# Optimization experiments

Hardware: AMD Instinct MI355X
Metric: run time of the kernel (lower is better)

## Reference

```python
import jax, jax.numpy as jnp
import numpy as np

N, E, B = 50000, 400000, 8
ND, ED, H, L = 32, 16, 128, 3

def setup_inputs() -> dict:
    key = jax.random.key(0)
    ks = jax.random.split(key, 32)
    s = 0.05
    inp = {
        'x': jax.random.normal(ks[0], (N, ND), jnp.float32),
        'edge_attr': jax.random.normal(ks[1], (E, ED), jnp.float32),
        'global_feature': jax.random.normal(ks[2], (B, 1), jnp.float32),
        'edge_index': jax.random.randint(ks[3], (2, E), 0, N, jnp.int64),
        'batch': jnp.sort(jax.random.randint(ks[4], (N,), 0, B, jnp.int64)),
        # embeddings
        'Wn': jax.random.normal(ks[5], (ND, H), jnp.float32) * s,
        'bn': jnp.zeros((H,), jnp.float32),
        'We': jax.random.normal(ks[6], (ED, H), jnp.float32) * s,
        'be': jnp.zeros((H,), jnp.float32),
        'Wg': jax.random.normal(ks[7], (1, H), jnp.float32) * s,
        'bg': jnp.zeros((H,), jnp.float32),
        # message-passing layers (stacked over L)
        'mW1': jax.random.normal(ks[8], (L, 3 * H, H), jnp.float32) * s,
        'mb1': jnp.zeros((L, H), jnp.float32),
        'mW2': jax.random.normal(ks[9], (L, H, H), jnp.float32) * s,
        'mb2': jnp.zeros((L, H), jnp.float32),
        'uW1': jax.random.normal(ks[10], (L, 2 * H, H), jnp.float32) * s,
        'ub1': jnp.zeros((L, H), jnp.float32),
        'uW2': jax.random.normal(ks[11], (L, H, H), jnp.float32) * s,
        'ub2': jnp.zeros((L, H), jnp.float32),
        # readout MLP
        'rW1': jax.random.normal(ks[12], (2 * H, H), jnp.float32) * s,
        'rb1': jnp.zeros((H,), jnp.float32),
        'rW2': jax.random.normal(ks[13], (H, H // 2), jnp.float32) * s,
        'rb2': jnp.zeros((H // 2,), jnp.float32),
        'rW3': jax.random.normal(ks[14], (H // 2, 1), jnp.float32) * s,
        'rb3': jnp.zeros((1,), jnp.float32),
    }
    return inp

def reference(x, edge_attr, global_feature, Wn, bn, We, be, Wg, bg,
              mW1, mb1, mW2, mb2, uW1, ub1, uW2, ub2,
              rW1, rb1, rW2, rb2, rW3, rb3, edge_index, batch):
    h = x @ Wn + bn                      # [N,H]
    e = edge_attr @ We + be              # [E,H]
    g = global_feature @ Wg + bg         # [B,H]
    src, dst = edge_index[0], edge_index[1]  # PyG: x_j=source, x_i=target, aggregate at target
    for l in range(L):
        m_in = jnp.concatenate([h[dst], h[src], e], axis=1)            # [E,3H]
        m = jax.nn.relu(m_in @ mW1[l] + mb1[l]) @ mW2[l] + mb2[l]       # [E,H]
        aggr = jax.ops.segment_sum(m, dst, num_segments=N)              # [N,H]
        u_in = jnp.concatenate([h, aggr], axis=1)                       # [N,2H]
        upd = jax.nn.relu(u_in @ uW1[l] + ub1[l]) @ uW2[l] + ub2[l]
        h = h + upd
    counts = jax.ops.segment_sum(jnp.ones((N,), h.dtype), batch, num_segments=B)
    pooled = jax.ops.segment_sum(h, batch, num_segments=B) / jnp.maximum(counts, 1.0)[:, None]
    final = jnp.concatenate([pooled, g], axis=1)                        # [B,2H]
    out = jax.nn.relu(final @ rW1 + rb1)
    out = jax.nn.relu(out @ rW2 + rb2)
    return out @ rW3 + rb3                                              # [B,1]
```

## Files before the change

kernel.cpp:

```cpp
#include <hip/hip_runtime.h>

#define NN 50000
#define NPAD 50048
#define NBLK 391
#define NE 400000
#define NBATCH 8
#define NDIM 32
#define EDIM 16
#define H 128
#define NLAYERS 3
#define CHUNK_ELEMS 4096
#define NODE_CHUNKS 24
#define ZW_CHUNK 8192
#define NSB 196

typedef __attribute__((ext_vector_type(8))) __bf16 bf16x8;
typedef __attribute__((ext_vector_type(16))) float f32x16;
typedef __attribute__((ext_vector_type(8))) short short8;
typedef __attribute__((ext_vector_type(2))) float v2f;

__device__ __forceinline__ void block_sync_lds() {
  asm volatile("s_waitcnt lgkmcnt(0)\ns_barrier" ::: "memory");
}
__device__ __forceinline__ v2f bf2f(unsigned u) {
  v2f r;
  r.x = __uint_as_float(u << 16);
  r.y = __uint_as_float(u & 0xffff0000u);
  return r;
}
__device__ __forceinline__ v2f fma2(float s, v2f w, v2f t) {
  v2f sv = {s, s};
  return __builtin_elementwise_fma(sv, w, t);
}

__global__ __launch_bounds__(128) void embed_nodes_kernel(
    const float* __restrict__ x, const float* __restrict__ Wn,
    const float* __restrict__ bn, __bf16* __restrict__ hb) {
  __shared__ float Ws[NDIM * H];
  __shared__ float xs[16 * NDIM];
  int j = threadIdx.x;
  int nbase = blockIdx.x * 16;
  for (int r = 0; r < NDIM; ++r) Ws[r * H + j] = Wn[r * H + j];
#pragma unroll
  for (int t = 0; t < 4; ++t) {
    int f = j + t * 128;
    xs[f] = x[nbase * NDIM + f];
  }
  __syncthreads();
  float b = bn[j];
  for (int nn = 0; nn < 16; ++nn) {
    float acc = b;
#pragma unroll
    for (int k = 0; k < NDIM; ++k)
      acc = fmaf(xs[nn * NDIM + k], Ws[k * H + j], acc);
    hb[(size_t)(nbase + nn) * H + j] = (__bf16)acc;
  }
}

__global__ __launch_bounds__(256) void degree_kernel(const int* __restrict__ ei,
                                                     int* __restrict__ deg) {
  int e = blockIdx.x * 256 + threadIdx.x;
  if (e < NE) atomicAdd(&deg[ei[NE + e]], 1);
}

__global__ __launch_bounds__(256) void scan1_kernel(const int* __restrict__ deg,
                                                    int* __restrict__ bsum) {
  __shared__ int ws[4];
  int i = blockIdx.x * 256 + threadIdx.x;
  int lane = threadIdx.x & 63, wid = threadIdx.x >> 6;
  int v = (i < NN) ? deg[i] : 0;
#pragma unroll
  for (int off = 32; off; off >>= 1) v += __shfl_down(v, off);
  if (lane == 0) ws[wid] = v;
  __syncthreads();
  if (threadIdx.x == 0) bsum[blockIdx.x] = ws[0] + ws[1] + ws[2] + ws[3];
}

__global__ __launch_bounds__(256) void scan2_kernel(const int* __restrict__ bsum,
                                                    int* __restrict__ boff) {
  __shared__ int s[256];
  int t = threadIdx.x;
  int v = (t < NSB) ? bsum[t] : 0;
  s[t] = v;
  __syncthreads();
  for (int off = 1; off < 256; off <<= 1) {
    int u = (t >= off) ? s[t - off] : 0;
    __syncthreads();
    s[t] += u;
    __syncthreads();
  }
  if (t < NSB) boff[t] = s[t] - v;
}

__global__ __launch_bounds__(256) void scan3_kernel(const int* __restrict__ deg,
                                                    const int* __restrict__ boff,
                                                    int* __restrict__ cursor) {
  __shared__ int wsum[4], woff[4];
  int i = blockIdx.x * 256 + threadIdx.x;
  int lane = threadIdx.x & 63, wid = threadIdx.x >> 6;
  int orig = (i < NN) ? deg[i] : 0;
  int v = orig;
#pragma unroll
  for (int off = 1; off < 64; off <<= 1) {
    int u = __shfl_up(v, off);
    if (lane >= off) v += u;
  }
  if (lane == 63) wsum[wid] = v;
  __syncthreads();
  if (threadIdx.x == 0) {
    int r = 0;
#pragma unroll
    for (int w = 0; w < 4; ++w) {
      woff[w] = r;
      r += wsum[w];
    }
  }
  __syncthreads();
  if (i < NN) cursor[i] = (v - orig) + woff[wid] + boff[blockIdx.x];
}

__global__ __launch_bounds__(256) void scatter_kernel(
    const int* __restrict__ ei, int* __restrict__ cursor,
    int2* __restrict__ seSrt) {
  int e = blockIdx.x * 256 + threadIdx.x;
  if (e < NE) {
    int d = ei[NE + e];
    int pos = atomicAdd(&cursor[d], 1);
    seSrt[pos] = make_int2(ei[e], e);
  }
}

__global__ __launch_bounds__(256) void gather_eaF_kernel(
    const float* __restrict__ ea, const int2* __restrict__ seSrt,
    float* __restrict__ eaF) {
  int fl = blockIdx.x * 256 + threadIdx.x;
  if (fl < NE) {
    int e = seSrt[fl].y;
    const float4* ep = (const float4*)(ea + (size_t)e * EDIM);
    float4* op = (float4*)(eaF + (size_t)fl * EDIM);
#pragma unroll
    for (int q = 0; q < 4; ++q) op[q] = ep[q];
  }
}

__global__ __launch_bounds__(256) void precomp_zw_kernel(
    const float* __restrict__ mW1, __bf16* __restrict__ ZW) {
  int l = blockIdx.x / 8;
  int c = blockIdx.x % 8;
  int tid = threadIdx.x;
  const float* w1 = mW1 + (size_t)l * 384 * H;
  __bf16* dst = ZW + ((size_t)l * 8 + c) * ZW_CHUNK;
  for (int it = 0; it < 32; ++it) {
    int flat = it * 256 + tid;
    int j = flat & 7;
    int lane = (flat >> 3) & 63;
    int nt = (flat >> 9) & 7;
    int hilo = flat >> 12;
    int k = c * 16 + ((lane >> 5) << 3) + j;
    int n = nt * 32 + (lane & 31);
    float w = (n < 128) ? w1[(size_t)k * H + n]
                        : w1[(size_t)(128 + k) * H + (n - 128)];
    __bf16 hi = (__bf16)w;
    __bf16 lo = (__bf16)(w - (float)hi);
    dst[flat] = hilo ? lo : hi;
  }
}

__global__ __launch_bounds__(128) void precomp_wef_kernel(
    const float* __restrict__ mW1, const float* __restrict__ mb1,
    const float* __restrict__ We, const float* __restrict__ be,
    float* __restrict__ Wef, float* __restrict__ bm) {
  int l = blockIdx.x;
  int n = threadIdx.x;
  const float* w1 = mW1 + (size_t)l * 384 * H;
  float acc[EDIM];
#pragma unroll
  for (int i = 0; i < EDIM; ++i) acc[i] = 0.f;
  float accb = 0.f;
  for (int c = 0; c < H; ++c) {
    float wv = w1[(size_t)(256 + c) * H + n];
    accb = fmaf(be[c], wv, accb);
#pragma unroll
    for (int i = 0; i < EDIM; ++i)
      acc[i] = fmaf(We[i * H + c], wv, acc[i]);
  }
#pragma unroll
  for (int i = 0; i < EDIM; ++i)
    Wef[((size_t)l * EDIM + i) * H + n] = acc[i];
  bm[l * H + n] = mb1[l * H + n] + accb;
}

__global__ __launch_bounds__(128) void precomp_wu_kernel(
    const float* __restrict__ uW1, const float* __restrict__ mW2,
    const float* __restrict__ mb2, float* __restrict__ Wu,
    float* __restrict__ va) {
  int l = blockIdx.x / 257;
  int r = blockIdx.x % 257;
  int j = threadIdx.x;
  const float* u1 = uW1 + (size_t)l * 256 * H;
  if (r < 128) {
    Wu[((size_t)l * 256 + r) * H + j] = u1[(size_t)r * H + j];
  } else if (r < 256) {
    int i = r - 128;
    const float* m2 = mW2 + ((size_t)l * H + i) * H;
    float s = 0.f;
    for (int c = 0; c < H; ++c)
      s = fmaf(m2[c], u1[(size_t)(128 + c) * H + j], s);
    Wu[((size_t)l * 256 + r) * H + j] = s;
  } else {
    float s = 0.f;
    for (int c = 0; c < H; ++c)
      s = fmaf(mb2[l * H + c], u1[(size_t)(128 + c) * H + j], s);
    va[l * H + j] = s;
  }
}

__global__ __launch_bounds__(256) void precomp_wns_kernel(
    const float* __restrict__ Wu, const float* __restrict__ uW2,
    __bf16* __restrict__ WnS) {
  int l = blockIdx.x / NODE_CHUNKS;
  int c = blockIdx.x % NODE_CHUNKS;
  int tid = threadIdx.x;
  int nt = tid >> 6, lane = tid & 63;
  int n = nt * 32 + (lane & 31);
  int half = lane >> 5;
  __bf16* dst = WnS + ((size_t)l * NODE_CHUNKS + c) * CHUNK_ELEMS;
#pragma unroll
  for (int j = 0; j < 8; ++j) {
    float w;
    if (c < 16) {
      int k = c * 16 + half * 8 + j;
      w = Wu[((size_t)l * 256 + k) * H + n];
    } else {
      int k = (c - 16) * 16 + half * 8 + j;
      w = uW2[((size_t)l * H + k) * H + n];
    }
    __bf16 hi = (__bf16)w;
    __bf16 lo = (__bf16)(w - (float)hi);
    dst[((0 * 4 + nt) * 64 + lane) * 8 + j] = hi;
    dst[((1 * 4 + nt) * 64 + lane) * 8 + j] = lo;
  }
}

__global__ __launch_bounds__(256) void zdzs_kernel(
    const __bf16* __restrict__ hb, const __bf16* __restrict__ ZW,
    const float* __restrict__ bm, __bf16* __restrict__ z) {
  __shared__ __align__(16) __bf16 Bt[2][ZW_CHUNK];
  int tid = threadIdx.x;
  int wid = tid >> 6, lane = tid & 63, m = lane & 31, half = lane >> 5;
  int nb = blockIdx.x * 128;
  int row = nb + wid * 32 + m;
  const __bf16* aH = hb + (size_t)row * H + half * 8;
  const short8* gW = (const short8*)ZW;
  short8* sB0 = (short8*)&Bt[0][0];
  short8* sB1 = (short8*)&Bt[1][0];
#pragma unroll
  for (int q = 0; q < 4; ++q) sB0[tid + q * 256] = gW[tid + q * 256];
  short8 p0 = gW[1024 + tid], p1 = gW[1024 + tid + 256];
  short8 p2 = gW[1024 + tid + 512], p3 = gW[1024 + tid + 768];
  f32x16 acc[8];
#pragma unroll
  for (int nt = 0; nt < 8; ++nt)
#pragma unroll
    for (int r = 0; r < 16; ++r) acc[nt][r] = 0.f;
  bf16x8 a = *(const bf16x8*)aH;
  block_sync_lds();

  for (int s = 0; s < 8; ++s) {
    int buf = s & 1;
    bf16x8 na = a;
    if (s + 1 < 8) na = *(const bf16x8*)(aH + (s + 1) * 16);
    if (s + 1 < 8) {
      short8* sb = buf ? sB0 : sB1;
      sb[tid] = p0;
      sb[tid + 256] = p1;
      sb[tid + 512] = p2;
      sb[tid + 768] = p3;
      if (s + 2 < 8) {
        p0 = gW[(size_t)(s + 2) * 1024 + tid];
        p1 = gW[(size_t)(s + 2) * 1024 + tid + 256];
        p2 = gW[(size_t)(s + 2) * 1024 + tid + 512];
        p3 = gW[(size_t)(s + 2) * 1024 + tid + 768];
      }
    }
    const __bf16* bb = &Bt[buf][0];
#pragma unroll
    for (int nt = 0; nt < 8; ++nt) {
      bf16x8 bh = *(const bf16x8*)&bb[((0 * 8 + nt) * 64 + lane) * 8];
      bf16x8 bl = *(const bf16x8*)&bb[((1 * 8 + nt) * 64 + lane) * 8];
      acc[nt] = __builtin_amdgcn_mfma_f32_32x32x16_bf16(a, bh, acc[nt], 0, 0, 0);
      acc[nt] = __builtin_amdgcn_mfma_f32_32x32x16_bf16(a, bl, acc[nt], 0, 0, 0);
    }
    a = na;
    if (s + 1 < 8) block_sync_lds();
  }

  float bmv[4];
#pragma unroll
  for (int nt = 0; nt < 4; ++nt) bmv[nt] = bm[nt * 32 + m];
#pragma unroll
  for (int nt = 0; nt < 8; ++nt) {
    float bias = (nt < 4) ? bmv[nt] : 0.f;
#pragma unroll
    for (int r = 0; r < 16; ++r) {
      int rowi = (r & 3) + 8 * (r >> 2) + 4 * half;
      z[(size_t)(nb + wid * 32 + rowi) * 256 + nt * 32 + m] =
          (__bf16)(acc[nt][r] + bias);
    }
  }
}

__global__ __launch_bounds__(256) void edge_aggr_kernel(
    const __bf16* __restrict__ z, const int2* __restrict__ seSrt,
    const int* __restrict__ cend, const float* __restrict__ eaF,
    const float* __restrict__ WefL, __bf16* __restrict__ aggrB) {
  __shared__ float wefS[EDIM * H];
  int tid = threadIdx.x;
#pragma unroll
  for (int q = 0; q < 8; ++q) wefS[tid + q * 256] = WefL[tid + q * 256];
  __syncthreads();
  int node = blockIdx.x * 4 + (tid >> 6);
  int lane = tid & 63;
  int c0 = lane * 2;
  v2f wef[16];
#pragma unroll
  for (int k = 0; k < 16; ++k) wef[k] = *(const v2f*)(&wefS[k * H + c0]);
  int end = cend[node];
  int start = node ? cend[node - 1] : 0;
  v2f acc = {0.f, 0.f};
  if (start < end) {
    v2f zd = bf2f(*(const unsigned*)(z + (size_t)node * 256 + c0));
    int sArr[4];
#pragma unroll
    for (int p = 0; p < 4; ++p)
      if (start + p < end) sArr[p] = seSrt[start + p].x;
    for (int e0 = start; e0 < end; e0 += 4) {
      unsigned zsb[4];
      float4 ea0[4], ea1[4], ea2[4], ea3[4];
#pragma unroll
      for (int p = 0; p < 4; ++p) {
        if (e0 + p < end) {
          zsb[p] = *(const unsigned*)(z + (size_t)sArr[p] * 256 + 128 + c0);
          const float4* ep = (const float4*)(eaF + (size_t)(e0 + p) * EDIM);
          ea0[p] = ep[0]; ea1[p] = ep[1]; ea2[p] = ep[2]; ea3[p] = ep[3];
        }
      }
#pragma unroll
      for (int p = 0; p < 4; ++p)
        if (e0 + 4 + p < end) sArr[p] = seSrt[e0 + 4 + p].x;
#pragma unroll
      for (int p = 0; p < 4; ++p) {
        if (e0 + p < end) {
          v2f t = zd + bf2f(zsb[p]);
          t = fma2(ea0[p].x, wef[0], t);
          t = fma2(ea0[p].y, wef[1], t);
          t = fma2(ea0[p].z, wef[2], t);
          t = fma2(ea0[p].w, wef[3], t);
          t = fma2(ea1[p].x, wef[4], t);
          t = fma2(ea1[p].y, wef[5], t);
          t = fma2(ea1[p].z, wef[6], t);
          t = fma2(ea1[p].w, wef[7], t);
          t = fma2(ea2[p].x, wef[8], t);
          t = fma2(ea2[p].y, wef[9], t);
          t = fma2(ea2[p].z, wef[10], t);
          t = fma2(ea2[p].w, wef[11], t);
          t = fma2(ea3[p].x, wef[12], t);
          t = fma2(ea3[p].y, wef[13], t);
          t = fma2(ea3[p].z, wef[14], t);
          t = fma2(ea3[p].w, wef[15], t);
          acc.x += fmaxf(t.x, 0.f);
          acc.y += fmaxf(t.y, 0.f);
        }
      }
    }
  }
  union { __bf16 b[2]; unsigned u; } pk;
  pk.b[0] = (__bf16)acc.x;
  pk.b[1] = (__bf16)acc.y;
  *(unsigned*)(aggrB + (size_t)node * H + c0) = pk.u;
}

__global__ __launch_bounds__(256) void node_update_mfma_kernel(
    __bf16* __restrict__ hb, const __bf16* __restrict__ aggrB,
    const int* __restrict__ deg, const __bf16* __restrict__ WnS,
    const float* __restrict__ ub1, const float* __restrict__ va,
    const float* __restrict__ ub2) {
  __shared__ __align__(16) __bf16 Bt[2][CHUNK_ELEMS];
  __shared__ __bf16 hid[2][32][132];
  __shared__ float degS[64];
  int tid = threadIdx.x;
  int nb = blockIdx.x * 64;
  if (tid < 64) degS[tid] = (float)deg[nb + tid];
  int wid = tid >> 6, lane = tid & 63, m = lane & 31, half = lane >> 5;
  int rg = wid & 1;
  int nh = wid >> 1;
  int row = nb + rg * 32 + m;
  const __bf16* aHb = hb + (size_t)row * H + half * 8;
  const __bf16* aGb = aggrB + (size_t)row * H + half * 8;
  const short8* gW = (const short8*)WnS;
  short8* sB0 = (short8*)&Bt[0][0];
  short8* sB1 = (short8*)&Bt[1][0];
  sB0[tid] = gW[tid];
  sB0[tid + 256] = gW[tid + 256];
  short8 p0 = gW[512 + tid], p1 = gW[512 + tid + 256];
  float bv1[2], bva[2];
#pragma unroll
  for (int ntl = 0; ntl < 2; ++ntl) {
    int nt = nh * 2 + ntl;
    bv1[ntl] = ub1[nt * 32 + m];
    bva[ntl] = va[nt * 32 + m];
  }
  f32x16 acc[2];
#pragma unroll
  for (int ntl = 0; ntl < 2; ++ntl)
#pragma unroll
    for (int r = 0; r < 16; ++r) acc[ntl][r] = 0.f;
  bf16x8 acur = *(const bf16x8*)aHb;
  block_sync_lds();

  for (int s = 0; s < 16; ++s) {
    int buf = s & 1;
    bf16x8 anext = acur;
    if (s + 1 < 16) {
      int sp = s + 1;
      anext = (sp < 8) ? *(const bf16x8*)(aHb + sp * 16)
                       : *(const bf16x8*)(aGb + (sp - 8) * 16);
    }
    {
      short8* sb = buf ? sB0 : sB1;
      sb[tid] = p0;
      sb[tid + 256] = p1;
      if (s + 2 < NODE_CHUNKS) {
        p0 = gW[(size_t)(s + 2) * 512 + tid];
        p1 = gW[(size_t)(s + 2) * 512 + tid + 256];
      }
    }
    const __bf16* bb = &Bt[buf][0];
#pragma unroll
    for (int ntl = 0; ntl < 2; ++ntl) {
      int nt = nh * 2 + ntl;
      bf16x8 bh = *(const bf16x8*)&bb[((0 * 4 + nt) * 64 + lane) * 8];
      bf16x8 bl = *(const bf16x8*)&bb[((1 * 4 + nt) * 64 + lane) * 8];
      acc[ntl] = __builtin_amdgcn_mfma_f32_32x32x16_bf16(acur, bh, acc[ntl], 0, 0, 0);
      acc[ntl] = __builtin_amdgcn_mfma_f32_32x32x16_bf16(acur, bl, acc[ntl], 0, 0, 0);
    }
    acur = anext;
    block_sync_lds();
  }

#pragma unroll
  for (int ntl = 0; ntl < 2; ++ntl) {
    int nt = nh * 2 + ntl;
#pragma unroll
    for (int r = 0; r < 16; ++r) {
      int rowi = (r & 3) + 8 * (r >> 2) + 4 * half;
      float v = acc[ntl][r] + bv1[ntl] + degS[rg * 32 + rowi] * bva[ntl];
      hid[rg][rowi][nt * 32 + m] = (__bf16)fmaxf(v, 0.f);
      acc[ntl][r] = 0.f;
    }
  }
  block_sync_lds();

  for (int s = 16; s < NODE_CHUNKS; ++s) {
    int buf = s & 1;
    if (s + 1 < NODE_CHUNKS) {
      short8* sb = buf ? sB0 : sB1;
      sb[tid] = p0;
      sb[tid + 256] = p1;
      if (s + 2 < NODE_CHUNKS) {
        p0 = gW[(size_t)(s + 2) * 512 + tid];
        p1 = gW[(size_t)(s + 2) * 512 + tid + 256];
      }
    }
    bf16x8 ah = *(const bf16x8*)&hid[rg][m][(s - 16) * 16 + half * 8];
    const __bf16* bb = &Bt[buf][0];
#pragma unroll
    for (int ntl = 0; ntl < 2; ++ntl) {
      int nt = nh * 2 + ntl;
      bf16x8 bh = *(const bf16x8*)&bb[((0 * 4 + nt) * 64 + lane) * 8];
      bf16x8 bl = *(const bf16x8*)&bb[((1 * 4 + nt) * 64 + lane) * 8];
      acc[ntl] = __builtin_amdgcn_mfma_f32_32x32x16_bf16(ah, bh, acc[ntl], 0, 0, 0);
      acc[ntl] = __builtin_amdgcn_mfma_f32_32x32x16_bf16(ah, bl, acc[ntl], 0, 0, 0);
    }
    if (s + 1 < NODE_CHUNKS) block_sync_lds();
  }

#pragma unroll
  for (int ntl = 0; ntl < 2; ++ntl) {
    int nt = nh * 2 + ntl;
    float b2 = ub2[nt * 32 + m];
#pragma unroll
    for (int r = 0; r < 16; ++r) {
      int rowi = (r & 3) + 8 * (r >> 2) + 4 * half;
      size_t idx = (size_t)(nb + rg * 32 + rowi) * H + nt * 32 + m;
      float hv = (float)hb[idx];
      hb[idx] = (__bf16)(hv + acc[ntl][r] + b2);
    }
  }
}

__global__ __launch_bounds__(256) void pool_kernel(
    const __bf16* __restrict__ hb, const int* __restrict__ batch,
    float* __restrict__ pooled, int* __restrict__ counts) {
  __shared__ float pS[NBATCH * H];
  __shared__ int cS[NBATCH];
  int tid = threadIdx.x;
  for (int i = tid; i < NBATCH * H; i += 256) pS[i] = 0.f;
  if (tid < NBATCH) cS[tid] = 0;
  __syncthreads();
  int c = tid & 15;
  int r0 = tid >> 4;
  int nbase = blockIdx.x * 128;
  v2f acc4[4] = {{0.f, 0.f}, {0.f, 0.f}, {0.f, 0.f}, {0.f, 0.f}};
  int cnt = 0;
  int cur = -1;
#pragma unroll
  for (int i = 0; i < 8; ++i) {
    int n = nbase + i * 16 + r0;
    if (n >= NN) break;
    int b = batch[n];
    if (b != cur) {
      if (cur >= 0) {
#pragma unroll
        for (int q = 0; q < 4; ++q) {
          atomicAdd(&pS[cur * H + c * 8 + q * 2], acc4[q].x);
          atomicAdd(&pS[cur * H + c * 8 + q * 2 + 1], acc4[q].y);
          acc4[q].x = 0.f;
          acc4[q].y = 0.f;
        }
        if (c == 0) atomicAdd(&cS[cur], cnt);
        cnt = 0;
      }
      cur = b;
    }
    uint4 v = *(const uint4*)(hb + (size_t)n * H + c * 8);
    acc4[0] += bf2f(v.x);
    acc4[1] += bf2f(v.y);
    acc4[2] += bf2f(v.z);
    acc4[3] += bf2f(v.w);
    cnt++;
  }
  if (cur >= 0) {
#pragma unroll
    for (int q = 0; q < 4; ++q) {
      atomicAdd(&pS[cur * H + c * 8 + q * 2], acc4[q].x);
      atomicAdd(&pS[cur * H + c * 8 + q * 2 + 1], acc4[q].y);
    }
    if (c == 0) atomicAdd(&cS[cur], cnt);
  }
  __syncthreads();
  for (int i = tid; i < NBATCH * H; i += 256) {
    float v = pS[i];
    if (v != 0.f) unsafeAtomicAdd(&pooled[i], v);
  }
  if (tid < NBATCH) {
    int cv = cS[tid];
    if (cv) atomicAdd(&counts[tid], cv);
  }
}

__global__ __launch_bounds__(128) void readout_kernel(
    const float* __restrict__ pooled, const int* __restrict__ counts,
    const float* __restrict__ gf, const float* __restrict__ Wg,
    const float* __restrict__ bg, const float* __restrict__ rW1,
    const float* __restrict__ rb1, const float* __restrict__ rW2,
    const float* __restrict__ rb2, const float* __restrict__ rW3,
    const float* __restrict__ rb3, float* __restrict__ out) {
  __shared__ float fin[256];
  __shared__ float t1[128];
  __shared__ float t2[64];
  int j = threadIdx.x;
  int b = blockIdx.x;
  float cnt = (float)counts[b];
  if (cnt < 1.f) cnt = 1.f;
  fin[j] = pooled[b * H + j] / cnt;
  fin[H + j] = fmaf(gf[b], Wg[j], bg[j]);
  __syncthreads();
  float a = rb1[j];
  for (int k = 0; k < 256; ++k) a = fmaf(fin[k], rW1[k * H + j], a);
  t1[j] = fmaxf(a, 0.f);
  __syncthreads();
  if (j < 64) {
    float a2 = rb2[j];
    for (int k = 0; k < 128; ++k) a2 = fmaf(t1[k], rW2[k * 64 + j], a2);
    t2[j] = fmaxf(a2, 0.f);
  }
  __syncthreads();
  if (j < 64) {
    float p = t2[j] * rW3[j];
#pragma unroll
    for (int off = 32; off; off >>= 1) p += __shfl_down(p, off);
    if (j == 0) out[b] = p + rb3[0];
  }
}

extern "C" void kernel_launch(void* const* d_in, const int* in_sizes, int n_in,
                              void* d_out, int out_size, void* d_ws, size_t ws_size,
                              hipStream_t stream) {
  const float* x   = (const float*)d_in[0];
  const float* ea  = (const float*)d_in[1];
  const float* gf  = (const float*)d_in[2];
  const int*   ei  = (const int*)d_in[3];
  const int*   bat = (const int*)d_in[4];
  const float* Wn  = (const float*)d_in[5];
  const float* bn  = (const float*)d_in[6];
  const float* We  = (const float*)d_in[7];
  const float* be  = (const float*)d_in[8];
  const float* Wg  = (const float*)d_in[9];
  const float* bg  = (const float*)d_in[10];
  const float* mW1 = (const float*)d_in[11];
  const float* mb1 = (const float*)d_in[12];
  const float* mW2 = (const float*)d_in[13];
  const float* mb2 = (const float*)d_in[14];
  const float* uW1 = (const float*)d_in[15];
  const float* ub1 = (const float*)d_in[16];
  const float* uW2 = (const float*)d_in[17];
  const float* ub2 = (const float*)d_in[18];
  const float* rW1 = (const float*)d_in[19];
  const float* rb1 = (const float*)d_in[20];
  const float* rW2 = (const float*)d_in[21];
  const float* rb2 = (const float*)d_in[22];
  const float* rW3 = (const float*)d_in[23];
  const float* rb3 = (const float*)d_in[24];

  char* p = (char*)d_ws;
  __bf16* hb     = (__bf16*)p; p += (size_t)NPAD * H * 2;
  __bf16* aggrB  = (__bf16*)p; p += (size_t)NPAD * H * 2;
  __bf16* z      = (__bf16*)p; p += (size_t)NPAD * 256 * 2;
  float*  eaF    = (float*)p;  p += (size_t)NE * EDIM * 4;
  int2*   seSrt  = (int2*)p;   p += (size_t)NE * 8;
  __bf16* ZW     = (__bf16*)p; p += (size_t)NLAYERS * 8 * ZW_CHUNK * 2;
  __bf16* WnS    = (__bf16*)p; p += (size_t)NLAYERS * NODE_CHUNKS * CHUNK_ELEMS * 2;
  float*  Wef    = (float*)p;  p += (size_t)NLAYERS * EDIM * H * 4;
  float*  bm     = (float*)p;  p += (size_t)NLAYERS * H * 4;
  float*  Wu     = (float*)p;  p += (size_t)NLAYERS * 256 * H * 4;
  float*  va     = (float*)p;  p += (size_t)NLAYERS * H * 4;
  int*    deg    = (int*)p;    p += (size_t)NPAD * 4;
  int*    cursor = (int*)p;    p += (size_t)NPAD * 4;
  int*    bsum   = (int*)p;    p += 256 * 4;
  int*    boff   = (int*)p;    p += 256 * 4;
  float*  pooled = (float*)p;  p += (size_t)NBATCH * H * 4;
  int*    counts = (int*)p;    p += 64;

  hipMemsetAsync(deg, 0, (size_t)NPAD * 4, stream);
  hipMemsetAsync(cursor, 0, (size_t)NPAD * 4, stream);
  hipMemsetAsync(pooled, 0, (size_t)NBATCH * H * 4, stream);
  hipMemsetAsync(counts, 0, 64, stream);

  embed_nodes_kernel<<<NN / 16, 128, 0, stream>>>(x, Wn, bn, hb);
  degree_kernel<<<(NE + 255) / 256, 256, 0, stream>>>(ei, deg);
  scan1_kernel<<<NSB, 256, 0, stream>>>(deg, bsum);
  scan2_kernel<<<1, 256, 0, stream>>>(bsum, boff);
  scan3_kernel<<<NSB, 256, 0, stream>>>(deg, boff, cursor);
  scatter_kernel<<<(NE + 255) / 256, 256, 0, stream>>>(ei, cursor, seSrt);
  gather_eaF_kernel<<<(NE + 255) / 256, 256, 0, stream>>>(ea, seSrt, eaF);
  precomp_zw_kernel<<<NLAYERS * 8, 256, 0, stream>>>(mW1, ZW);
  precomp_wef_kernel<<<NLAYERS, 128, 0, stream>>>(mW1, mb1, We, be, Wef, bm);
  precomp_wu_kernel<<<NLAYERS * 257, 128, 0, stream>>>(uW1, mW2, mb2, Wu, va);
  precomp_wns_kernel<<<NLAYERS * NODE_CHUNKS, 256, 0, stream>>>(Wu, uW2, WnS);

  for (int l = 0; l < NLAYERS; ++l) {
    zdzs_kernel<<<NBLK, 256, 0, stream>>>(
        hb, ZW + (size_t)l * 8 * ZW_CHUNK, bm + (size_t)l * H, z);
    edge_aggr_kernel<<<NPAD / 4, 256, 0, stream>>>(
        z, seSrt, cursor, eaF, Wef + (size_t)l * EDIM * H, aggrB);
    node_update_mfma_kernel<<<NPAD / 64, 256, 0, stream>>>(
        hb, aggrB, deg, WnS + (size_t)l * NODE_CHUNKS * CHUNK_ELEMS,
        ub1 + (size_t)l * H, va + (size_t)l * H, ub2 + (size_t)l * H);
  }

  pool_kernel<<<NPAD / 128, 256, 0, stream>>>(hb, bat, pooled, counts);
  readout_kernel<<<NBATCH, 128, 0, stream>>>(pooled, counts, gf, Wg, bg, rW1,
                                             rb1, rW2, rb2, rW3, rb3,
                                             (float*)d_out);
}
```

Before: 584.5 us.

## Switch edge aggregation to edge-balanced waves with segmented atomic flush

Edge aggregation now gives each wave a fixed run of 64 dst-sorted edges instead of one destination node, so per-wave work is balanced regardless of node degree. Partial segments at a wave's edges are merged with float atomics into an fp32 aggregate buffer, which is zeroed with a memset every layer. The node update reads the fp32 aggregate and converts it to bf16 on load. This adds a memset, doubles the aggregate traffic and introduces atomics in exchange for removing the imbalance from variable degree.

```diff
diff --git a/kernel.cpp b/kernel.cpp
--- a/kernel.cpp
+++ b/kernel.cpp
@@ -13,6 +13,8 @@
 #define NODE_CHUNKS 24
 #define ZW_CHUNK 8192
 #define NSB 196
+#define EPW 64
+#define EAB 1563
 
 typedef __attribute__((ext_vector_type(8))) __bf16 bf16x8;
 typedef __attribute__((ext_vector_type(16))) float f32x16;
@@ -121,21 +123,22 @@
 
 __global__ __launch_bounds__(256) void scatter_kernel(
     const int* __restrict__ ei, int* __restrict__ cursor,
-    int2* __restrict__ seSrt) {
+    int2* __restrict__ sdSrt, int* __restrict__ eidSrt) {
   int e = blockIdx.x * 256 + threadIdx.x;
   if (e < NE) {
     int d = ei[NE + e];
     int pos = atomicAdd(&cursor[d], 1);
-    seSrt[pos] = make_int2(ei[e], e);
+    sdSrt[pos] = make_int2(ei[e], d);
+    eidSrt[pos] = e;
   }
 }
 
 __global__ __launch_bounds__(256) void gather_eaF_kernel(
-    const float* __restrict__ ea, const int2* __restrict__ seSrt,
+    const float* __restrict__ ea, const int* __restrict__ eidSrt,
     float* __restrict__ eaF) {
   int fl = blockIdx.x * 256 + threadIdx.x;
   if (fl < NE) {
-    int e = seSrt[fl].y;
+    int e = eidSrt[fl];
     const float4* ep = (const float4*)(ea + (size_t)e * EDIM);
     float4* op = (float4*)(eaF + (size_t)fl * EDIM);
 #pragma unroll
@@ -310,78 +313,85 @@
   }
 }
 
+__device__ __forceinline__ void flush_seg(float* __restrict__ aggrF, int d,
+                                          int c0, v2f acc, bool partial) {
+  if (partial) {
+    unsafeAtomicAdd(&aggrF[(size_t)d * H + c0], acc.x);
+    unsafeAtomicAdd(&aggrF[(size_t)d * H + c0 + 1], acc.y);
+  } else {
+    *(v2f*)(&aggrF[(size_t)d * H + c0]) = acc;
+  }
+}
+
 __global__ __launch_bounds__(256) void edge_aggr_kernel(
-    const __bf16* __restrict__ z, const int2* __restrict__ seSrt,
-    const int* __restrict__ cend, const float* __restrict__ eaF,
-    const float* __restrict__ WefL, __bf16* __restrict__ aggrB) {
+    const __bf16* __restrict__ z, const int2* __restrict__ sdSrt,
+    const float* __restrict__ eaF, const float* __restrict__ WefL,
+    float* __restrict__ aggrF) {
   __shared__ float wefS[EDIM * H];
   int tid = threadIdx.x;
 #pragma unroll
   for (int q = 0; q < 8; ++q) wefS[tid + q * 256] = WefL[tid + q * 256];
   __syncthreads();
-  int node = blockIdx.x * 4 + (tid >> 6);
   int lane = tid & 63;
   int c0 = lane * 2;
+  int wave = blockIdx.x * 4 + (tid >> 6);
+  int e0 = wave * EPW;
+  if (e0 >= NE) return;
   v2f wef[16];
 #pragma unroll
   for (int k = 0; k < 16; ++k) wef[k] = *(const v2f*)(&wefS[k * H + c0]);
-  int end = cend[node];
-  int start = node ? cend[node - 1] : 0;
+
+  int curD = sdSrt[e0].y;
+  v2f zdv = bf2f(*(const unsigned*)(z + (size_t)curD * 256 + c0));
   v2f acc = {0.f, 0.f};
-  if (start < end) {
-    v2f zd = bf2f(*(const unsigned*)(z + (size_t)node * 256 + c0));
-    int sArr[4];
-#pragma unroll
-    for (int p = 0; p < 4; ++p)
-      if (start + p < end) sArr[p] = seSrt[start + p].x;
-    for (int e0 = start; e0 < end; e0 += 4) {
-      unsigned zsb[4];
-      float4 ea0[4], ea1[4], ea2[4], ea3[4];
-#pragma unroll
-      for (int p = 0; p < 4; ++p) {
-        if (e0 + p < end) {
-          zsb[p] = *(const unsigned*)(z + (size_t)sArr[p] * 256 + 128 + c0);
-          const float4* ep = (const float4*)(eaF + (size_t)(e0 + p) * EDIM);
-          ea0[p] = ep[0]; ea1[p] = ep[1]; ea2[p] = ep[2]; ea3[p] = ep[3];
-        }
+  bool firstSeg = true;
+
+  for (int b = e0; b < e0 + EPW; b += 8) {
+    int2 sd[8];
+#pragma unroll
+    for (int p = 0; p < 8; ++p) sd[p] = sdSrt[b + p];
+    unsigned zsb[8];
+#pragma unroll
+    for (int p = 0; p < 8; ++p)
+      zsb[p] = *(const unsigned*)(z + (size_t)sd[p].x * 256 + 128 + c0);
+#pragma unroll
+    for (int p = 0; p < 8; ++p) {
+      if (sd[p].y != curD) {
+        flush_seg(aggrF, curD, c0, acc, firstSeg);
+        firstSeg = false;
+        acc.x = 0.f;
+        acc.y = 0.f;
+        curD = sd[p].y;
+        zdv = bf2f(*(const unsigned*)(z + (size_t)curD * 256 + c0));
       }
-#pragma unroll
-      for (int p = 0; p < 4; ++p)
-        if (e0 + 4 + p < end) sArr[p] = seSrt[e0 + 4 + p].x;
-#pragma unroll
-      for (int p = 0; p < 4; ++p) {
-        if (e0 + p < end) {
-          v2f t = zd + bf2f(zsb[p]);
-          t = fma2(ea0[p].x, wef[0], t);
-          t = fma2(ea0[p].y, wef[1], t);
-          t = fma2(ea0[p].z, wef[2], t);
-          t = fma2(ea0[p].w, wef[3], t);
-          t = fma2(ea1[p].x, wef[4], t);
-          t = fma2(ea1[p].y, wef[5], t);
-          t = fma2(ea1[p].z, wef[6], t);
-          t = fma2(ea1[p].w, wef[7], t);
-          t = fma2(ea2[p].x, wef[8], t);
-          t = fma2(ea2[p].y, wef[9], t);
-          t = fma2(ea2[p].z, wef[10], t);
-          t = fma2(ea2[p].w, wef[11], t);
-          t = fma2(ea3[p].x, wef[12], t);
-          t = fma2(ea3[p].y, wef[13], t);
-          t = fma2(ea3[p].z, wef[14], t);
-          t = fma2(ea3[p].w, wef[15], t);
-          acc.x += fmaxf(t.x, 0.f);
-          acc.y += fmaxf(t.y, 0.f);
-        }
-      }
-    }
-  }
-  union { __bf16 b[2]; unsigned u; } pk;
-  pk.b[0] = (__bf16)acc.x;
-  pk.b[1] = (__bf16)acc.y;
-  *(unsigned*)(aggrB + (size_t)node * H + c0) = pk.u;
+      const float4* ep = (const float4*)(eaF + (size_t)(b + p) * EDIM);
+      float4 a0 = ep[0], a1 = ep[1], a2 = ep[2], a3 = ep[3];
+      v2f t = zdv + bf2f(zsb[p]);
+      t = fma2(a0.x, wef[0], t);
+      t = fma2(a0.y, wef[1], t);
+      t = fma2(a0.z, wef[2], t);
+      t = fma2(a0.w, wef[3], t);
+      t = fma2(a1.x, wef[4], t);
+      t = fma2(a1.y, wef[5], t);
+      t = fma2(a1.z, wef[6], t);
+      t = fma2(a1.w, wef[7], t);
+      t = fma2(a2.x, wef[8], t);
+      t = fma2(a2.y, wef[9], t);
+      t = fma2(a2.z, wef[10], t);
+      t = fma2(a2.w, wef[11], t);
+      t = fma2(a3.x, wef[12], t);
+      t = fma2(a3.y, wef[13], t);
+      t = fma2(a3.z, wef[14], t);
+      t = fma2(a3.w, wef[15], t);
+      acc.x += fmaxf(t.x, 0.f);
+      acc.y += fmaxf(t.y, 0.f);
+    }
+  }
+  flush_seg(aggrF, curD, c0, acc, true);
 }
 
 __global__ __launch_bounds__(256) void node_update_mfma_kernel(
-    __bf16* __restrict__ hb, const __bf16* __restrict__ aggrB,
+    __bf16* __restrict__ hb, const float* __restrict__ aggrF,
     const int* __restrict__ deg, const __bf16* __restrict__ WnS,
     const float* __restrict__ ub1, const float* __restrict__ va,
     const float* __restrict__ ub2) {
@@ -396,7 +406,7 @@
   int nh = wid >> 1;
   int row = nb + rg * 32 + m;
   const __bf16* aHb = hb + (size_t)row * H + half * 8;
-  const __bf16* aGb = aggrB + (size_t)row * H + half * 8;
+  const float* aG = aggrF + (size_t)row * H + half * 8;
   const short8* gW = (const short8*)WnS;
   short8* sB0 = (short8*)&Bt[0][0];
   short8* sB1 = (short8*)&Bt[1][0];
@@ -423,8 +433,16 @@
     bf16x8 anext = acur;
     if (s + 1 < 16) {
       int sp = s + 1;
-      anext = (sp < 8) ? *(const bf16x8*)(aHb + sp * 16)
-                       : *(const bf16x8*)(aGb + (sp - 8) * 16);
+      if (sp < 8) {
+        anext = *(const bf16x8*)(aHb + sp * 16);
+      } else {
+        const float* pp = aG + (sp - 8) * 16;
+        float4 f0 = *(const float4*)pp;
+        float4 f1 = *(const float4*)(pp + 4);
+        float af[8] = {f0.x, f0.y, f0.z, f0.w, f1.x, f1.y, f1.z, f1.w};
+#pragma unroll
+        for (int j = 0; j < 8; ++j) anext[j] = (__bf16)af[j];
+      }
     }
     {
       short8* sb = buf ? sB0 : sB1;
@@ -625,10 +643,11 @@
 
   char* p = (char*)d_ws;
   __bf16* hb     = (__bf16*)p; p += (size_t)NPAD * H * 2;
-  __bf16* aggrB  = (__bf16*)p; p += (size_t)NPAD * H * 2;
+  float*  aggrF  = (float*)p;  p += (size_t)NPAD * H * 4;
   __bf16* z      = (__bf16*)p; p += (size_t)NPAD * 256 * 2;
   float*  eaF    = (float*)p;  p += (size_t)NE * EDIM * 4;
-  int2*   seSrt  = (int2*)p;   p += (size_t)NE * 8;
+  int2*   sdSrt  = (int2*)p;   p += (size_t)NE * 8;
+  int*    eidSrt = (int*)p;    p += (size_t)NE * 4;
   __bf16* ZW     = (__bf16*)p; p += (size_t)NLAYERS * 8 * ZW_CHUNK * 2;
   __bf16* WnS    = (__bf16*)p; p += (size_t)NLAYERS * NODE_CHUNKS * CHUNK_ELEMS * 2;
   float*  Wef    = (float*)p;  p += (size_t)NLAYERS * EDIM * H * 4;
@@ -652,8 +671,8 @@
   scan1_kernel<<<NSB, 256, 0, stream>>>(deg, bsum);
   scan2_kernel<<<1, 256, 0, stream>>>(bsum, boff);
   scan3_kernel<<<NSB, 256, 0, stream>>>(deg, boff, cursor);
-  scatter_kernel<<<(NE + 255) / 256, 256, 0, stream>>>(ei, cursor, seSrt);
-  gather_eaF_kernel<<<(NE + 255) / 256, 256, 0, stream>>>(ea, seSrt, eaF);
+  scatter_kernel<<<(NE + 255) / 256, 256, 0, stream>>>(ei, cursor, sdSrt, eidSrt);
+  gather_eaF_kernel<<<(NE + 255) / 256, 256, 0, stream>>>(ea, eidSrt, eaF);
   precomp_zw_kernel<<<NLAYERS * 8, 256, 0, stream>>>(mW1, ZW);
   precomp_wef_kernel<<<NLAYERS, 128, 0, stream>>>(mW1, mb1, We, be, Wef, bm);
   precomp_wu_kernel<<<NLAYERS * 257, 128, 0, stream>>>(uW1, mW2, mb2, Wu, va);
@@ -662,10 +681,11 @@
   for (int l = 0; l < NLAYERS; ++l) {
     zdzs_kernel<<<NBLK, 256, 0, stream>>>(
         hb, ZW + (size_t)l * 8 * ZW_CHUNK, bm + (size_t)l * H, z);
-    edge_aggr_kernel<<<NPAD / 4, 256, 0, stream>>>(
-        z, seSrt, cursor, eaF, Wef + (size_t)l * EDIM * H, aggrB);
+    hipMemsetAsync(aggrF, 0, (size_t)NPAD * H * 4, stream);
+    edge_aggr_kernel<<<EAB, 256, 0, stream>>>(
+        z, sdSrt, eaF, Wef + (size_t)l * EDIM * H, aggrF);
     node_update_mfma_kernel<<<NPAD / 64, 256, 0, stream>>>(
-        hb, aggrB, deg, WnS + (size_t)l * NODE_CHUNKS * CHUNK_ELEMS,
+        hb, aggrF, deg, WnS + (size_t)l * NODE_CHUNKS * CHUNK_ELEMS,
         ub1 + (size_t)l * H, va + (size_t)l * H, ub2 + (size_t)l * H);
   }
 
```

Measured after the change: 614.5 us. 1.05x slower.
